# Kernel tuning notes

Measured on AMD Instinct MI355X. Metric: run time of the kernel, lower is better.

The kernel has to match this reference:

```python
import jax, jax.numpy as jnp
import numpy as np

B = 131072          # points on manifold
A = 16              # n_anchors
SDIM = 512          # substrate.n (spatial dim); ambient dim = SDIM + 1
ALPHA = 0.1         # attraction coefficient
EPS = 1e-7


def _proj(p):
    # Project onto hyperboloid: recompute time coord from spatial part.
    sp = p[..., 1:]
    t = jnp.sqrt(1.0 + jnp.sum(sp * sp, axis=-1, keepdims=True))
    return jnp.concatenate([t, sp], axis=-1)


def _linner(x, y):
    # Lorentz inner product <x,y>_L = -x0*y0 + sum_i xi*yi
    return -x[..., 0] * y[..., 0] + jnp.sum(x[..., 1:] * y[..., 1:], axis=-1)


def setup_inputs() -> dict:
    key = jax.random.key(0)
    k1, k2 = jax.random.split(key)
    x_sp = jax.random.normal(k1, (B, SDIM), dtype=jnp.float32)
    x = _proj(jnp.concatenate([jnp.zeros((B, 1), jnp.float32), x_sp], axis=-1))
    a_sp = jax.random.normal(k2, (A, SDIM), dtype=jnp.float32) * 0.01
    anchors = _proj(jnp.concatenate([jnp.zeros((A, 1), jnp.float32), a_sp], axis=-1))
    return {"x": x, "anchors": anchors}


def reference(x, anchors):
    af = _proj(anchors)                                   # [A, D]
    D = af.shape[-1]
    metric = jnp.concatenate([-jnp.ones((1,), x.dtype), jnp.ones((D - 1,), x.dtype)])
    # pairwise -<x,a>_L  -> [B, A]
    theta_all = -jnp.einsum('bd,ad->ba', x * metric, af)
    dists = jnp.arccosh(jnp.clip(theta_all, 1.0 + EPS, None))
    idx = jnp.argmin(dists, axis=1)                       # nearest anchor per point
    y = af[idx]                                           # [B, D]
    # log_map_x(y) = acosh(theta)/sqrt(theta^2-1) * (y - theta*x)
    theta = jnp.clip(-_linner(x, y), 1.0 + EPS, None)[:, None]
    direction = (jnp.arccosh(theta) / jnp.sqrt(theta * theta - 1.0)) * (y - theta * x)
    v = ALPHA * direction                                 # tangent vector
    # exp_map_x(v) = cosh(||v||_L) x + sinh(||v||_L)/||v||_L * v
    vn = jnp.sqrt(jnp.clip(_linner(v, v), EPS, None))[:, None]
    return jnp.cosh(vn) * x + (jnp.sinh(vn) / vn) * v
```

## Files before the change

### kernel.cpp

```cpp
#include <hip/hip_runtime.h>

#define B_ROWS 131072
#define NA 16
#define DD 513
#define ALPHA 0.1f
#define EPSV 1e-7f

__global__ __launch_bounds__(256, 2)
void hfield_kernel(const float* __restrict__ x,
                   const float* __restrict__ anc,
                   float* __restrict__ out) {
    __shared__ float lds_af[NA * DD];
    __shared__ __attribute__((aligned(16))) float redbuf[4][64 * 20];

    const int tid  = threadIdx.x;
    const int lane = tid & 63;
    const int wid  = tid >> 6;
    const int gw   = blockIdx.x * 4 + wid;
    const int TW   = gridDim.x * 4;

    for (int i = tid; i < NA * DD; i += 256) lds_af[i] = anc[i];

    float Areg[NA][8];
#pragma unroll
    for (int a = 0; a < NA; ++a) {
#pragma unroll
        for (int j = 0; j < 8; ++j)
            Areg[a][j] = anc[a * DD + 1 + lane + 64 * j];
    }

    float* wb = redbuf[wid];
    const int g     = lane >> 4;
    const int amine = lane & 15;

    float af0;
    {
        float q[NA];
#pragma unroll
        for (int a = 0; a < NA; ++a) {
            float s = 0.f;
#pragma unroll
            for (int j = 0; j < 8; ++j) s = fmaf(Areg[a][j], Areg[a][j], s);
            q[a] = s;
        }
#pragma unroll
        for (int t4 = 0; t4 < 4; ++t4)
            *reinterpret_cast<float4*>(&wb[lane * 20 + 4 * t4]) =
                make_float4(q[4 * t4], q[4 * t4 + 1], q[4 * t4 + 2], q[4 * t4 + 3]);
        asm volatile("s_waitcnt lgkmcnt(0)" ::: "memory");
        float t = 0.f;
#pragma unroll
        for (int k = 0; k < 16; ++k) t += wb[(g + 4 * k) * 20 + amine];
        t += __shfl_xor(t, 16);
        t += __shfl_xor(t, 32);
        af0 = sqrtf(1.0f + t);
    }

    __syncthreads();

    const float thmin = 1.0f + 1e-7f;

    int row = gw;
    float xn[8], x0n = 0.f;
    if (row < B_ROWS) {
        const float* rp = x + (size_t)row * DD;
        x0n = rp[0];
#pragma unroll
        for (int j = 0; j < 8; ++j) xn[j] = rp[1 + lane + 64 * j];
    }

    for (; row < B_ROWS; row += TW) {
        float xc[8];
        const float x0 = x0n;
#pragma unroll
        for (int j = 0; j < 8; ++j) xc[j] = xn[j];

        const int nrow = row + TW;
        if (nrow < B_ROWS) {
            const float* rp = x + (size_t)nrow * DD;
            x0n = rp[0];
#pragma unroll
            for (int j = 0; j < 8; ++j) xn[j] = rp[1 + lane + 64 * j];
        }

        float q[NA];
#pragma unroll
        for (int a = 0; a < NA; ++a) {
            float s = 0.f;
#pragma unroll
            for (int j = 0; j < 8; ++j) s = fmaf(xc[j], Areg[a][j], s);
            q[a] = s;
        }

#pragma unroll
        for (int t4 = 0; t4 < 4; ++t4)
            *reinterpret_cast<float4*>(&wb[lane * 20 + 4 * t4]) =
                make_float4(q[4 * t4], q[4 * t4 + 1], q[4 * t4 + 2], q[4 * t4 + 3]);
        asm volatile("s_waitcnt lgkmcnt(0)" ::: "memory");
        float t = 0.f;
#pragma unroll
        for (int k = 0; k < 16; ++k) t += wb[(g + 4 * k) * 20 + amine];
        t += __shfl_xor(t, 16);
        t += __shfl_xor(t, 32);

        float tc = fmaxf(fmaf(x0, af0, -t), thmin);
        int   bi = amine;

#pragma unroll
        for (int m = 1; m <= 8; m <<= 1) {
            float vo = __shfl_xor(tc, m);
            int   io = __shfl_xor(bi, m);
            bool take = (vo < tc) || (vo == tc && io < bi);
            tc = take ? vo : tc;
            bi = take ? io : bi;
        }

        float s2   = tc * tc - 1.0f;
        float rr   = sqrtf(s2);
        float ach  = logf(tc + rr);
        float coef = ach / rr;
        float vn   = sqrtf(fmaxf(ALPHA * ALPHA * ach * ach, EPSV));
        float e    = expf(vn);
        float ei   = 1.0f / e;
        float ch   = 0.5f * (e + ei);
        float sh   = 0.5f * (e - ei);
        float c2   = ALPHA * coef * (sh / vn);
        float c1   = fmaf(-c2, tc, ch);

        float* op = out + (size_t)row * DD;
        const float* yp = lds_af + bi * DD + 1 + lane;
#pragma unroll
        for (int j = 0; j < 8; ++j) {
            float y = yp[64 * j];
            __builtin_nontemporal_store(fmaf(c2, y, c1 * xc[j]), &op[1 + lane + 64 * j]);
        }
        float y0   = __shfl(af0, bi);
        float out0 = fmaf(c2, y0, c1 * x0);
        if (lane == 0) __builtin_nontemporal_store(out0, &op[0]);
    }
}

extern "C" void kernel_launch(void* const* d_in, const int* in_sizes, int n_in,
                              void* d_out, int out_size, void* d_ws, size_t ws_size,
                              hipStream_t stream) {
    const float* x   = (const float*)d_in[0];
    const float* anc = (const float*)d_in[1];
    float* out       = (float*)d_out;
    hipLaunchKernelGGL(hfield_kernel, dim3(1024), dim3(256), 0, stream, x, anc, out);
}
```

Baseline: 116.2 us.

## Gather nearest anchor from registers instead of LDS copy, pad reduction buffer

Drops the shared-memory copy of all anchors and the block barrier. The nearest-anchor row is now selected from register-resident anchor data through a wave-uniform switch on readfirstlane(bi), which frees about 32KB of LDS per block. The reduction buffer pitch changes from 20 to 17 with scalar stores to reduce bank conflicts, and logf/expf are replaced by the fast __logf/__expf intrinsics. Risks are register pressure from the switch and a small loss of accuracy in the transcendentals.

```diff
diff --git a/kernel.cpp b/kernel.cpp
--- a/kernel.cpp
+++ b/kernel.cpp
@@ -5,13 +5,13 @@
 #define DD 513
 #define ALPHA 0.1f
 #define EPSV 1e-7f
+#define PITCH 17
 
 __global__ __launch_bounds__(256, 2)
 void hfield_kernel(const float* __restrict__ x,
                    const float* __restrict__ anc,
                    float* __restrict__ out) {
-    __shared__ float lds_af[NA * DD];
-    __shared__ __attribute__((aligned(16))) float redbuf[4][64 * 20];
+    __shared__ float redbuf[4][64 * PITCH];
 
     const int tid  = threadIdx.x;
     const int lane = tid & 63;
@@ -19,15 +19,18 @@
     const int gw   = blockIdx.x * 4 + wid;
     const int TW   = gridDim.x * 4;
 
-    for (int i = tid; i < NA * DD; i += 256) lds_af[i] = anc[i];
-
     float Areg[NA][8];
 #pragma unroll
-    for (int a = 0; a < NA; ++a) {
+    for (int a = 0; a < NA; ++a)
 #pragma unroll
         for (int j = 0; j < 8; ++j)
             Areg[a][j] = anc[a * DD + 1 + lane + 64 * j];
-    }
+
+#pragma unroll
+    for (int a = 0; a < NA; ++a)
+#pragma unroll
+        for (int j = 0; j < 8; ++j)
+            asm volatile("" : "+v"(Areg[a][j]));
 
     float* wb = redbuf[wid];
     const int g     = lane >> 4;
@@ -44,19 +47,15 @@
             q[a] = s;
         }
 #pragma unroll
-        for (int t4 = 0; t4 < 4; ++t4)
-            *reinterpret_cast<float4*>(&wb[lane * 20 + 4 * t4]) =
-                make_float4(q[4 * t4], q[4 * t4 + 1], q[4 * t4 + 2], q[4 * t4 + 3]);
+        for (int i = 0; i < NA; ++i) wb[lane * PITCH + i] = q[i];
         asm volatile("s_waitcnt lgkmcnt(0)" ::: "memory");
         float t = 0.f;
 #pragma unroll
-        for (int k = 0; k < 16; ++k) t += wb[(g + 4 * k) * 20 + amine];
+        for (int k = 0; k < 16; ++k) t += wb[(g + 4 * k) * PITCH + amine];
         t += __shfl_xor(t, 16);
         t += __shfl_xor(t, 32);
         af0 = sqrtf(1.0f + t);
     }
-
-    __syncthreads();
 
     const float thmin = 1.0f + 1e-7f;
 
@@ -93,13 +92,11 @@
         }
 
 #pragma unroll
-        for (int t4 = 0; t4 < 4; ++t4)
-            *reinterpret_cast<float4*>(&wb[lane * 20 + 4 * t4]) =
-                make_float4(q[4 * t4], q[4 * t4 + 1], q[4 * t4 + 2], q[4 * t4 + 3]);
+        for (int i = 0; i < NA; ++i) wb[lane * PITCH + i] = q[i];
         asm volatile("s_waitcnt lgkmcnt(0)" ::: "memory");
         float t = 0.f;
 #pragma unroll
-        for (int k = 0; k < 16; ++k) t += wb[(g + 4 * k) * 20 + amine];
+        for (int k = 0; k < 16; ++k) t += wb[(g + 4 * k) * PITCH + amine];
         t += __shfl_xor(t, 16);
         t += __shfl_xor(t, 32);
 
@@ -117,24 +114,33 @@
 
         float s2   = tc * tc - 1.0f;
         float rr   = sqrtf(s2);
-        float ach  = logf(tc + rr);
+        float ach  = __logf(tc + rr);
         float coef = ach / rr;
         float vn   = sqrtf(fmaxf(ALPHA * ALPHA * ach * ach, EPSV));
-        float e    = expf(vn);
+        float e    = __expf(vn);
         float ei   = 1.0f / e;
         float ch   = 0.5f * (e + ei);
         float sh   = 0.5f * (e - ei);
         float c2   = ALPHA * coef * (sh / vn);
         float c1   = fmaf(-c2, tc, ch);
 
+        const int bis = __builtin_amdgcn_readfirstlane(bi);
+        float y[8];
+        switch (bis) {
+#define YCASE(A) case A: _Pragma("unroll") for (int j = 0; j < 8; ++j) y[j] = Areg[A][j]; break;
+            YCASE(0)  YCASE(1)  YCASE(2)  YCASE(3)
+            YCASE(4)  YCASE(5)  YCASE(6)  YCASE(7)
+            YCASE(8)  YCASE(9)  YCASE(10) YCASE(11)
+            YCASE(12) YCASE(13) YCASE(14) YCASE(15)
+#undef YCASE
+        }
+
         float* op = out + (size_t)row * DD;
-        const float* yp = lds_af + bi * DD + 1 + lane;
 #pragma unroll
-        for (int j = 0; j < 8; ++j) {
-            float y = yp[64 * j];
-            __builtin_nontemporal_store(fmaf(c2, y, c1 * xc[j]), &op[1 + lane + 64 * j]);
-        }
-        float y0   = __shfl(af0, bi);
+        for (int j = 0; j < 8; ++j)
+            __builtin_nontemporal_store(fmaf(c2, y[j], c1 * xc[j]), &op[1 + lane + 64 * j]);
+
+        float y0   = __shfl(af0, bis);
         float out0 = fmaf(c2, y0, c1 * x0);
         if (lane == 0) __builtin_nontemporal_store(out0, &op[0]);
     }
```

Result: no change. 117.0 us (+0.6%).
